# Kernel optimization log

Measured on AMD Instinct MI355X. Metric: run time of the kernel, lower is better.

The kernel has to match this reference:

```python
import math
import jax, jax.numpy as jnp
import numpy as np

_TEMP_CLAMP = 4.6

def _l2n(x):
    # torch F.normalize: x / max(||x||, eps)
    return x / jnp.maximum(jnp.linalg.norm(x, axis=-1, keepdims=True), 1e-12)

def setup_inputs() -> dict:
    key = jax.random.key(0)
    k1, k2, k3, k4, k5 = jax.random.split(key, 5)
    B, S, D, V, NNEG = 1024, 64, 128, 100000, 2048
    hidden = jax.random.normal(k1, (B, S, D), dtype=jnp.float32)
    y = jax.random.randint(k2, (B, S), 0, V, dtype=jnp.int64)
    embed_table = jax.random.normal(k3, (V, D), dtype=jnp.float32)
    sampling_probs = jax.random.uniform(k4, (V,), dtype=jnp.float32, minval=1e-6, maxval=1.0)
    sampled_indices = jax.random.randint(k5, (NNEG,), 0, V, dtype=jnp.int64)
    log_temperature = jnp.asarray(math.log(1.0 / 0.07), dtype=jnp.float32)
    return {"hidden": hidden, "y": y, "embed_table": embed_table,
            "sampling_probs": sampling_probs, "sampled_indices": sampled_indices,
            "log_temperature": log_temperature}

def reference(hidden, y, embed_table, sampling_probs, sampled_indices, log_temperature):
    D = hidden.shape[-1]
    h = hidden.reshape(-1, D)          # [N, D]
    yf = y.reshape(-1)                 # [N]
    valid = (yf != 0)                  # padding mask (static-shape weighting instead of boolean gather)

    true_p = sampling_probs[yf]                # [N]
    samp_p = sampling_probs[sampled_indices]   # [NNEG]
    e_pos = embed_table[yf]                    # [N, D]
    e_neg = embed_table[sampled_indices]       # [NNEG, D]

    temp = jnp.exp(jnp.minimum(log_temperature, _TEMP_CLAMP))
    hn = _l2n(h)
    pos_logits = jnp.sum(hn * _l2n(e_pos), axis=-1) * temp        # [N]
    neg_logits = (hn @ _l2n(e_neg).T) * temp                      # [N, NNEG]

    collision = yf[:, None] == sampled_indices[None, :]
    neg_logits = jnp.where(collision, -1e9, neg_logits)

    pos_adj = pos_logits - jnp.log(true_p + 1e-10)                # [N]
    neg_adj = neg_logits - jnp.log(samp_p + 1e-10)[None, :]       # [N, NNEG]
    logits = jnp.concatenate([pos_adj[:, None], neg_adj], axis=1) # [N, 1+NNEG]

    per_row = -jax.nn.log_softmax(logits, axis=-1)[:, 0]          # CE with label 0
    w = valid.astype(per_row.dtype)
    return jnp.sum(per_row * w) / jnp.maximum(jnp.sum(w), 1.0)
```

## Files before the change

kernel.cpp:

```cpp
#include <hip/hip_runtime.h>
#include <math.h>

#define TPB 256
#define NNEG 2048
#define D 128
#define CHUNK 64
#define NCH (NNEG / CHUNK)
#define RPB 128
#define RPW 32
#define L2E 1.44269504088896340736f

typedef __attribute__((ext_vector_type(8))) short bf16x8;
typedef __attribute__((ext_vector_type(4))) float f32x4;

#define MFMA16 __builtin_amdgcn_mfma_f32_16x16x32_bf16

static __device__ __forceinline__ unsigned int f2bf(float f) {
    unsigned int u = __float_as_uint(f);
    return (u + 0x7FFFu + ((u >> 16) & 1u)) >> 16;
}

static __device__ __forceinline__ void stage16(const void* g, void* l) {
    __builtin_amdgcn_global_load_lds(
        (const __attribute__((address_space(1))) unsigned int*)g,
        (__attribute__((address_space(3))) unsigned int*)l, 16, 0, 0);
}

__global__ __launch_bounds__(TPB) void sspe_prep(
    const float* __restrict__ embed,
    const float* __restrict__ sprobs,
    const int* __restrict__ sidx,
    unsigned int* __restrict__ en_bf,
    float* __restrict__ ln_samp)
{
    const int t = threadIdx.x;
    const int wave = t >> 6;
    const int lane = t & 63;
    const int j = blockIdx.x * 4 + wave;
    const int idx = sidx[j];

    float2 v = reinterpret_cast<const float2*>(embed)[(size_t)idx * 64 + lane];
    float ss = v.x * v.x + v.y * v.y;
    ss += __shfl_xor(ss, 1);
    ss += __shfl_xor(ss, 2);
    ss += __shfl_xor(ss, 4);
    ss += __shfl_xor(ss, 8);
    ss += __shfl_xor(ss, 16);
    ss += __shfl_xor(ss, 32);
    const float rinv = 1.0f / fmaxf(sqrtf(ss), 1e-12f);
    en_bf[(size_t)j * 64 + lane] = f2bf(v.x * rinv) | (f2bf(v.y * rinv) << 16);
    if (lane == 0) ln_samp[j] = logf(sprobs[idx] + 1e-10f);
}

__global__ __launch_bounds__(TPB, 2) void sspe_main(
    const float* __restrict__ hidden,
    const int* __restrict__ y,
    const float* __restrict__ embed,
    const float* __restrict__ sprobs,
    const int* __restrict__ sidx,
    const float* __restrict__ ltemp,
    const unsigned int* __restrict__ en_bf,
    const float* __restrict__ ln_samp,
    float2* __restrict__ partials)
{
    const int t = threadIdx.x;
    const int wave = t >> 6;
    const int lane = t & 63;
    const int rb = blockIdx.x * RPB;

    __shared__ __align__(16) unsigned char smem[RPB * 256];
    __shared__ float pos_s[RPB];
    __shared__ int   ys[RPB];
    __shared__ float sums[RPB];
    __shared__ float2 red2[4];

    const float temp = __builtin_amdgcn_exp2f(fminf(ltemp[0], 4.6f) * L2E);
    const float t2 = temp * L2E;
    const float Mln = temp + 14.0f;
    const float M2 = Mln * L2E;

    if (t < RPB) ys[t] = y[rb + t];
    __syncthreads();

    #pragma unroll 1
    for (int i = 0; i < RPW; i += 4) {
        float2 h2[4], e2[4];
        int yi[4];
        #pragma unroll
        for (int u = 0; u < 4; ++u) {
            const int lr = wave * RPW + i + u;
            h2[u] = reinterpret_cast<const float2*>(hidden)[(size_t)(rb + lr) * 64 + lane];
            yi[u] = ys[lr];
        }
        #pragma unroll
        for (int u = 0; u < 4; ++u)
            e2[u] = reinterpret_cast<const float2*>(embed)[(size_t)yi[u] * 64 + lane];
        float ss[4], es[4], dt[4];
        #pragma unroll
        for (int u = 0; u < 4; ++u) {
            ss[u] = h2[u].x * h2[u].x + h2[u].y * h2[u].y;
            es[u] = e2[u].x * e2[u].x + e2[u].y * e2[u].y;
            dt[u] = h2[u].x * e2[u].x + h2[u].y * e2[u].y;
        }
        #pragma unroll
        for (int m = 1; m <= 32; m <<= 1)
            #pragma unroll
            for (int u = 0; u < 4; ++u) {
                ss[u] += __shfl_xor(ss[u], m);
                es[u] += __shfl_xor(es[u], m);
                dt[u] += __shfl_xor(dt[u], m);
            }
        #pragma unroll
        for (int u = 0; u < 4; ++u) {
            const int lr = wave * RPW + i + u;
            const float rinv = 1.0f / fmaxf(sqrtf(ss[u]), 1e-12f);
            const unsigned int uu = f2bf(h2[u].x * rinv) | (f2bf(h2[u].y * rinv) << 16);
            const int rx = (lr & 7) << 4;
            *reinterpret_cast<unsigned int*>(smem + lr * 256 + ((lane * 4) ^ rx)) = uu;
            if (lane == 0)
                pos_s[lr] = dt[u] * rinv * (1.0f / fmaxf(sqrtf(es[u]), 1e-12f)) * temp
                            - logf(sprobs[yi[u]] + 1e-10f);
        }
    }
    __syncthreads();

    bf16x8 A0[4], A1[4];
    {
        const int row0 = wave * RPW + (lane & 15);
        const int rx = (lane & 7) << 4;
        #pragma unroll
        for (int ks = 0; ks < 4; ++ks) {
            const int col = (ks * 64 + ((lane >> 4) << 4)) ^ rx;
            A0[ks] = *reinterpret_cast<const bf16x8*>(smem + row0 * 256 + col);
            A1[ks] = *reinterpret_cast<const bf16x8*>(smem + (row0 + 16) * 256 + col);
        }
    }
    __syncthreads();

    const int cj = lane & 15;
    const int rgrp = lane >> 4;
    int yv0[4], yv1[4];
    float l0[4], l1[4];
    #pragma unroll
    for (int j = 0; j < 4; ++j) {
        yv0[j] = ys[wave * RPW + rgrp * 4 + j];
        yv1[j] = ys[wave * RPW + 16 + rgrp * 4 + j];
        l0[j] = 0.0f;
        l1[j] = 0.0f;
    }

    unsigned int soff[4];
    #pragma unroll
    for (int i = 0; i < 4; ++i) {
        const int d = wave * 4 + i;
        soff[i] = (unsigned int)((d >> 2) * 4096 + (lane & 15) * 256
                                 + (d & 3) * 64 + (lane >> 4) * 16);
    }
    const unsigned char* en = reinterpret_cast<const unsigned char*>(en_bf);

    #pragma unroll
    for (int i = 0; i < 4; ++i)
        stage16(en + soff[i], smem + (wave * 4 + i) * 1024);

    #pragma unroll 1
    for (int ch = 0; ch < NCH; ++ch) {
        const int cur = (ch & 1) << 14;
        __syncthreads();

        float lk[4];
        int ci[4];
        #pragma unroll
        for (int nt = 0; nt < 4; ++nt) {
            lk[nt] = ln_samp[ch * 64 + nt * 16 + cj];
            ci[nt] = sidx[ch * 64 + nt * 16 + cj];
        }

        if (ch + 1 < NCH) {
            const unsigned char* enn = en + (size_t)(ch + 1) * 16384;
            #pragma unroll
            for (int i = 0; i < 4; ++i)
                stage16(enn + soff[i], smem + (cur ^ 16384) + (wave * 4 + i) * 1024);
        }

        const unsigned char* bb = smem + cur + lane * 16;
        f32x4 c0[4], c1[4];
        #pragma unroll
        for (int nt = 0; nt < 4; ++nt) {
            c0[nt] = (f32x4){0.f, 0.f, 0.f, 0.f};
            c1[nt] = (f32x4){0.f, 0.f, 0.f, 0.f};
            #pragma unroll
            for (int ks = 0; ks < 4; ++ks) {
                const bf16x8 b = *reinterpret_cast<const bf16x8*>(bb + (nt * 4 + ks) * 1024);
                c0[nt] = MFMA16(A0[ks], b, c0[nt], 0, 0, 0);
                c1[nt] = MFMA16(A1[ks], b, c1[nt], 0, 0, 0);
            }
        }

        #pragma unroll
        for (int nt = 0; nt < 4; ++nt) {
            const float nl2 = fmaf(lk[nt], -L2E, -M2);
            #pragma unroll
            for (int j = 0; j < 4; ++j) {
                const float a0 = fmaf(c0[nt][j], t2, nl2);
                const float a1 = fmaf(c1[nt][j], t2, nl2);
                const float e0 = __builtin_amdgcn_exp2f(a0);
                const float e1 = __builtin_amdgcn_exp2f(a1);
                l0[j] += (ci[nt] == yv0[j]) ? 0.0f : e0;
                l1[j] += (ci[nt] == yv1[j]) ? 0.0f : e1;
            }
        }
    }

    #pragma unroll
    for (int j = 0; j < 4; ++j) {
        float v0 = l0[j], v1 = l1[j];
        v0 += __shfl_xor(v0, 1);  v1 += __shfl_xor(v1, 1);
        v0 += __shfl_xor(v0, 2);  v1 += __shfl_xor(v1, 2);
        v0 += __shfl_xor(v0, 4);  v1 += __shfl_xor(v1, 4);
        v0 += __shfl_xor(v0, 8);  v1 += __shfl_xor(v1, 8);
        l0[j] = v0;
        l1[j] = v1;
    }
    if (cj == 0) {
        #pragma unroll
        for (int j = 0; j < 4; ++j) {
            sums[wave * RPW + rgrp * 4 + j] = l0[j];
            sums[wave * RPW + 16 + rgrp * 4 + j] = l1[j];
        }
    }
    __syncthreads();

    float per = 0.0f, w = 0.0f;
    if (t < RPB) {
        const float s = sums[t];
        const float pa = pos_s[t];
        const float stot = s + __builtin_amdgcn_exp2f(fmaf(pa, L2E, -M2));
        w = (ys[t] != 0) ? 1.0f : 0.0f;
        per = (Mln + logf(stot) - pa) * w;
    }
    #pragma unroll
    for (int msk = 1; msk < 64; msk <<= 1) {
        per += __shfl_xor(per, msk);
        w += __shfl_xor(w, msk);
    }
    if (lane == 0) red2[wave] = make_float2(per, w);
    __syncthreads();
    if (t == 0) {
        const float2 a = red2[0], b = red2[1], c = red2[2], d = red2[3];
        partials[blockIdx.x] = make_float2(a.x + b.x + c.x + d.x,
                                           a.y + b.y + c.y + d.y);
    }
}

__global__ __launch_bounds__(TPB) void sspe_finalize(
    const float2* __restrict__ partials, int n, float* __restrict__ out)
{
    __shared__ float ssum[TPB];
    __shared__ float scnt[TPB];
    const int t = threadIdx.x;
    float s = 0.0f, c = 0.0f;
    for (int i = t; i < n; i += TPB) {
        const float2 p = partials[i];
        s += p.x; c += p.y;
    }
    ssum[t] = s; scnt[t] = c;
    __syncthreads();
    for (int k = TPB / 2; k > 0; k >>= 1) {
        if (t < k) { ssum[t] += ssum[t + k]; scnt[t] += scnt[t + k]; }
        __syncthreads();
    }
    if (t == 0) out[0] = ssum[0] / fmaxf(scnt[0], 1.0f);
}

extern "C" void kernel_launch(void* const* d_in, const int* in_sizes, int n_in,
                              void* d_out, int out_size, void* d_ws, size_t ws_size,
                              hipStream_t stream) {
    const float* hidden = (const float*)d_in[0];
    const int*   yv     = (const int*)d_in[1];
    const float* embed  = (const float*)d_in[2];
    const float* sprobs = (const float*)d_in[3];
    const int*   sidx   = (const int*)d_in[4];
    const float* ltemp  = (const float*)d_in[5];
    float* out = (float*)d_out;

    const int nrows = in_sizes[1];
    const int nblocks = nrows / RPB;

    char* w = (char*)d_ws;
    unsigned int* en_bf  = (unsigned int*)w;
    float*  ln_samp      = (float*)(w + (size_t)NNEG * D * 2);
    float2* partials     = (float2*)(w + (size_t)NNEG * D * 2 + NNEG * 4);

    sspe_prep<<<NNEG / 4, TPB, 0, stream>>>(embed, sprobs, sidx, en_bf, ln_samp);
    sspe_main<<<nblocks, TPB, 0, stream>>>(hidden, yv, embed, sprobs, sidx, ltemp,
                                           en_bf, ln_samp, partials);
    sspe_finalize<<<1, TPB, 0, stream>>>(partials, nblocks, out);
}
```

Measured before the change: 95.82 us.

## Split negative samples across two blocks per row tile, add row-combine kernel

Each 128-row tile is now handled by two blocks, each covering half of the 2048 negatives, which doubles the grid (512 to 1024 blocks) and raises the launch-bounds occupancy hint to 4. Per-row partial exp-sums and positive logits go to workspace, and a new sspe_rows kernel combines them into per-block loss partials before finalize. The aim is better CU occupancy and latency hiding. The cost is that both blocks re-read and re-normalize the hidden rows, plus one extra kernel launch and extra global traffic.

```diff
diff --git a/kernel.cpp b/kernel.cpp
--- a/kernel.cpp
+++ b/kernel.cpp
@@ -4,10 +4,11 @@
 #define TPB 256
 #define NNEG 2048
 #define D 128
-#define CHUNK 64
-#define NCH (NNEG / CHUNK)
 #define RPB 128
 #define RPW 32
+#define NSPLIT 2
+#define HALF (NNEG / NSPLIT)
+#define NCHH (HALF / 64)
 #define L2E 1.44269504088896340736f
 
 typedef __attribute__((ext_vector_type(8))) short bf16x8;
@@ -52,7 +53,7 @@
     if (lane == 0) ln_samp[j] = logf(sprobs[idx] + 1e-10f);
 }
 
-__global__ __launch_bounds__(TPB, 2) void sspe_main(
+__global__ __launch_bounds__(TPB, 4) void sspe_main(
     const float* __restrict__ hidden,
     const int* __restrict__ y,
     const float* __restrict__ embed,
@@ -61,18 +62,18 @@
     const float* __restrict__ ltemp,
     const unsigned int* __restrict__ en_bf,
     const float* __restrict__ ln_samp,
-    float2* __restrict__ partials)
+    float* __restrict__ pos_adj,
+    float* __restrict__ lsum,
+    int nrows)
 {
     const int t = threadIdx.x;
     const int wave = t >> 6;
     const int lane = t & 63;
-    const int rb = blockIdx.x * RPB;
+    const int jh = blockIdx.x & 1;
+    const int rb = (blockIdx.x >> 1) * RPB;
 
     __shared__ __align__(16) unsigned char smem[RPB * 256];
-    __shared__ float pos_s[RPB];
-    __shared__ int   ys[RPB];
-    __shared__ float sums[RPB];
-    __shared__ float2 red2[4];
+    __shared__ int ys[RPB];
 
     const float temp = __builtin_amdgcn_exp2f(fminf(ltemp[0], 4.6f) * L2E);
     const float t2 = temp * L2E;
@@ -91,10 +92,13 @@
             const int lr = wave * RPW + i + u;
             h2[u] = reinterpret_cast<const float2*>(hidden)[(size_t)(rb + lr) * 64 + lane];
             yi[u] = ys[lr];
-        }
-        #pragma unroll
-        for (int u = 0; u < 4; ++u)
-            e2[u] = reinterpret_cast<const float2*>(embed)[(size_t)yi[u] * 64 + lane];
+            e2[u] = make_float2(0.0f, 0.0f);
+        }
+        if (jh == 0) {
+            #pragma unroll
+            for (int u = 0; u < 4; ++u)
+                e2[u] = reinterpret_cast<const float2*>(embed)[(size_t)yi[u] * 64 + lane];
+        }
         float ss[4], es[4], dt[4];
         #pragma unroll
         for (int u = 0; u < 4; ++u) {
@@ -117,9 +121,9 @@
             const unsigned int uu = f2bf(h2[u].x * rinv) | (f2bf(h2[u].y * rinv) << 16);
             const int rx = (lr & 7) << 4;
             *reinterpret_cast<unsigned int*>(smem + lr * 256 + ((lane * 4) ^ rx)) = uu;
-            if (lane == 0)
-                pos_s[lr] = dt[u] * rinv * (1.0f / fmaxf(sqrtf(es[u]), 1e-12f)) * temp
-                            - logf(sprobs[yi[u]] + 1e-10f);
+            if (jh == 0 && lane == 0)
+                pos_adj[rb + lr] = dt[u] * rinv * (1.0f / fmaxf(sqrtf(es[u]), 1e-12f)) * temp
+                                   - logf(sprobs[yi[u]] + 1e-10f);
         }
     }
     __syncthreads();
@@ -156,14 +160,16 @@
         soff[i] = (unsigned int)((d >> 2) * 4096 + (lane & 15) * 256
                                  + (d & 3) * 64 + (lane >> 4) * 16);
     }
-    const unsigned char* en = reinterpret_cast<const unsigned char*>(en_bf);
+    const unsigned char* en = reinterpret_cast<const unsigned char*>(en_bf)
+                            + (size_t)jh * HALF * 256;
+    const int nb0 = jh * HALF;
 
     #pragma unroll
     for (int i = 0; i < 4; ++i)
         stage16(en + soff[i], smem + (wave * 4 + i) * 1024);
 
     #pragma unroll 1
-    for (int ch = 0; ch < NCH; ++ch) {
+    for (int ch = 0; ch < NCHH; ++ch) {
         const int cur = (ch & 1) << 14;
         __syncthreads();
 
@@ -171,11 +177,11 @@
         int ci[4];
         #pragma unroll
         for (int nt = 0; nt < 4; ++nt) {
-            lk[nt] = ln_samp[ch * 64 + nt * 16 + cj];
-            ci[nt] = sidx[ch * 64 + nt * 16 + cj];
-        }
-
-        if (ch + 1 < NCH) {
+            lk[nt] = ln_samp[nb0 + ch * 64 + nt * 16 + cj];
+            ci[nt] = sidx[nb0 + ch * 64 + nt * 16 + cj];
+        }
+
+        if (ch + 1 < NCHH) {
             const unsigned char* enn = en + (size_t)(ch + 1) * 16384;
             #pragma unroll
             for (int i = 0; i < 4; ++i)
@@ -222,22 +228,39 @@
         l1[j] = v1;
     }
     if (cj == 0) {
+        float* dst = lsum + (size_t)jh * nrows + rb + wave * RPW;
         #pragma unroll
         for (int j = 0; j < 4; ++j) {
-            sums[wave * RPW + rgrp * 4 + j] = l0[j];
-            sums[wave * RPW + 16 + rgrp * 4 + j] = l1[j];
-        }
-    }
-    __syncthreads();
-
-    float per = 0.0f, w = 0.0f;
-    if (t < RPB) {
-        const float s = sums[t];
-        const float pa = pos_s[t];
-        const float stot = s + __builtin_amdgcn_exp2f(fmaf(pa, L2E, -M2));
-        w = (ys[t] != 0) ? 1.0f : 0.0f;
-        per = (Mln + logf(stot) - pa) * w;
-    }
+            dst[rgrp * 4 + j] = l0[j];
+            dst[16 + rgrp * 4 + j] = l1[j];
+        }
+    }
+}
+
+__global__ __launch_bounds__(TPB) void sspe_rows(
+    const int* __restrict__ y,
+    const float* __restrict__ ltemp,
+    const float* __restrict__ pos_adj,
+    const float* __restrict__ lsum,
+    int nrows,
+    float2* __restrict__ partials)
+{
+    __shared__ float2 red2[4];
+    const int t = threadIdx.x;
+    const int wave = t >> 6;
+    const int lane = t & 63;
+    const int r = blockIdx.x * TPB + t;
+
+    const float temp = __builtin_amdgcn_exp2f(fminf(ltemp[0], 4.6f) * L2E);
+    const float Mln = temp + 14.0f;
+    const float M2 = Mln * L2E;
+
+    const float s = lsum[r] + lsum[(size_t)nrows + r];
+    const float pa = pos_adj[r];
+    const float stot = s + __builtin_amdgcn_exp2f(fmaf(pa, L2E, -M2));
+    float w = (y[r] != 0) ? 1.0f : 0.0f;
+    float per = (Mln + logf(stot) - pa) * w;
+
     #pragma unroll
     for (int msk = 1; msk < 64; msk <<= 1) {
         per += __shfl_xor(per, msk);
@@ -284,15 +307,19 @@
     float* out = (float*)d_out;
 
     const int nrows = in_sizes[1];
-    const int nblocks = nrows / RPB;
+    const int nblocks = (nrows / RPB) * NSPLIT;
 
     char* w = (char*)d_ws;
-    unsigned int* en_bf  = (unsigned int*)w;
-    float*  ln_samp      = (float*)(w + (size_t)NNEG * D * 2);
-    float2* partials     = (float2*)(w + (size_t)NNEG * D * 2 + NNEG * 4);
+    size_t off = 0;
+    unsigned int* en_bf = (unsigned int*)(w + off); off += (size_t)NNEG * D * 2;
+    float* ln_samp      = (float*)(w + off);        off += (size_t)NNEG * 4;
+    float* pos_adj      = (float*)(w + off);        off += (size_t)nrows * 4;
+    float* lsum         = (float*)(w + off);        off += (size_t)NSPLIT * nrows * 4;
+    float2* partials    = (float2*)(w + off);
 
     sspe_prep<<<NNEG / 4, TPB, 0, stream>>>(embed, sprobs, sidx, en_bf, ln_samp);
     sspe_main<<<nblocks, TPB, 0, stream>>>(hidden, yv, embed, sprobs, sidx, ltemp,
-                                           en_bf, ln_samp, partials);
-    sspe_finalize<<<1, TPB, 0, stream>>>(partials, nblocks, out);
-}
+                                           en_bf, ln_samp, pos_adj, lsum, nrows);
+    sspe_rows<<<nrows / TPB, TPB, 0, stream>>>(yv, ltemp, pos_adj, lsum, nrows, partials);
+    sspe_finalize<<<1, TPB, 0, stream>>>(partials, nrows / TPB, out);
+}
```

Result: faster. 93.72 us (-2.2%).
